# Kernel tuning notes

Hardware: AMD Instinct MI355X
Metric: run time of the kernel (lower is better)

## Reference

```python
import jax, jax.numpy as jnp
import numpy as np

N, E, H, OUT, L = 50000, 500000, 256, 128, 2
EPS = 1e-5  # torch LayerNorm default


def _make_edges(k):
    # both rows cover all N nodes so that unique()/remap in the original is identity
    k1, k2, kp = jax.random.split(k, 3)
    row0 = jnp.concatenate([jax.random.permutation(kp, N), jax.random.randint(k1, (E - N,), 0, N)])
    row1 = jnp.concatenate([jnp.arange(N), jax.random.randint(k2, (E - N,), 0, N)])
    return jnp.stack([row0, row1]).astype(jnp.int32)


def setup_inputs() -> dict:
    key = jax.random.key(0)
    ks = jax.random.split(key, 7)
    s = 0.02
    x = jax.random.normal(ks[0], (N, H), jnp.float32)
    edge_r1 = _make_edges(ks[1])
    edge_r2 = _make_edges(ks[2])
    Wl = jax.random.normal(ks[3], (L, H, H), jnp.float32) * s
    W0 = jax.random.normal(ks[4], (L, H, H), jnp.float32) * s
    W1 = jax.random.normal(ks[5], (L, H, H), jnp.float32) * s
    bl = jnp.zeros((L, H), jnp.float32)
    b0 = jnp.zeros((L, H), jnp.float32)
    b1 = jnp.zeros((L, H), jnp.float32)
    gamma = jnp.ones((L, H), jnp.float32)
    beta = jnp.zeros((L, H), jnp.float32)
    Wout = jax.random.normal(ks[6], (OUT, H), jnp.float32) * s
    bout = jnp.zeros((OUT,), jnp.float32)
    return dict(x=x, edge_r1=edge_r1, edge_r2=edge_r2, Wl=Wl, bl=bl, W0=W0, b0=b0,
                W1=W1, b1=b1, gamma=gamma, beta=beta, Wout=Wout, bout=bout)


def _layer(i, h, x0, e, Wl, bl, W0, b0, W1, b1, gamma, beta):
    # PyG flow='target_to_source', aggr='add': gather h at e[1], scatter-add at e[0]
    agg = jax.ops.segment_sum(h[e[1]], e[0], num_segments=h.shape[0])  # [N, H]
    z = agg @ Wl[i].T + bl[i] + h @ W0[i].T + b0[i] + x0 @ W1[i].T + b1[i]
    z = jax.nn.relu(z)
    mu = jnp.mean(z, axis=-1, keepdims=True)
    var = jnp.mean(jnp.square(z - mu), axis=-1, keepdims=True)
    return (z - mu) * jax.lax.rsqrt(var + EPS) * gamma[i] + beta[i]  # dropout is identity in eval


def reference(x, edge_r1, edge_r2, Wl, bl, W0, b0, W1, b1, gamma, beta, Wout, bout):
    # reversed(metapath): (C,r2,C) with conv_idx=1 first, then (C,r1,C) with conv_idx=0
    h = _layer(1, x, x, edge_r2, Wl, bl, W0, b0, W1, b1, gamma, beta)
    h = _layer(0, h, x, edge_r1, Wl, bl, W0, b0, W1, b1, gamma, beta)
    return h @ Wout.T + bout  # [N, OUT]
```

## Files before the change

### kernel.cpp

```cpp
#include <hip/hip_runtime.h>
#include <stdint.h>

#define N_NODES 50000
#define N_EDGES 500000
#define NPAD    50048
#define NBLK    128
#define EPB     4096
#define NBUCK   391
#define LFLAT   50048
#define NSC2    196
#define P4CAP   4096
#define EPS     1e-5f

typedef _Float16 half8_ __attribute__((ext_vector_type(8)));
typedef _Float16 half4_ __attribute__((ext_vector_type(4)));
typedef float    float4_ __attribute__((ext_vector_type(4)));

typedef uint32_t u32_g __attribute__((address_space(1)));
typedef uint32_t u32_s __attribute__((address_space(3)));

__device__ __forceinline__ void gload16(const void* g, void* lds_wave_base) {
    __builtin_amdgcn_global_load_lds((const u32_g*)g, (u32_s*)lds_wave_base, 16, 0, 0);
}

__global__ __launch_bounds__(256) void prep_kernel(
        const int* __restrict__ e1, const int* __restrict__ e2,
        int* __restrict__ G, unsigned short* __restrict__ rank16,
        const float* __restrict__ x, _Float16* __restrict__ xh,
        _Float16* __restrict__ aggb, _Float16* __restrict__ h1,
        const float* __restrict__ Wl, const float* __restrict__ W0,
        const float* __restrict__ W1, const float* __restrict__ Wout,
        _Float16* __restrict__ Wcat,
        const float* __restrict__ bl, const float* __restrict__ b0,
        const float* __restrict__ b1, const float* __restrict__ bout,
        float* __restrict__ bias) {
    __shared__ int hist[NBUCK];
    const int bid = blockIdx.x;
    const int tid = threadIdx.x;
    if (bid < 256) {
        const int s = bid >> 7, blk = bid & 127;
        const int* dst = s ? e2 : e1;
        unsigned short* rk = rank16 + (size_t)s * N_EDGES;
        for (int b = tid; b < NBUCK; b += 256) hist[b] = 0;
        __syncthreads();
        const int e0 = blk * EPB;
        int myrank[16];
#pragma unroll
        for (int k = 0; k < 16; k++) {
            int i = e0 + k * 256 + tid;
            int r = 0;
            if (i < N_EDGES) r = atomicAdd(&hist[dst[i] >> 7], 1);
            myrank[k] = r;
        }
#pragma unroll
        for (int k = 0; k < 16; k++) {
            int i = e0 + k * 256 + tid;
            if (i < N_EDGES) rk[i] = (unsigned short)myrank[k];
        }
        __syncthreads();
        int* Gp = G + (s * NBLK + blk) * NBUCK;
        for (int b = tid; b < NBUCK; b += 256) Gp[b] = hist[b];
    } else if (bid < 12756) {
        int i = (bid - 256) * 256 + tid;
        float4_ v = ((const float4_*)x)[i];
        half4_ h;
        h[0] = (_Float16)v[0]; h[1] = (_Float16)v[1];
        h[2] = (_Float16)v[2]; h[3] = (_Float16)v[3];
        ((half4_*)xh)[i] = h;
    } else if (bid < 14420) {
        int i = (bid - 12756) * 256 + tid;
        if (i < 2 * 256 * 768) {
            int l = i / (256 * 768);
            int r = i % (256 * 768);
            int j = r / 768, k = r % 768;
            const float* s = (k < 256) ? Wl : (k < 512 ? W0 : W1);
            Wcat[i] = (_Float16)s[l * 65536 + j * 256 + (k & 255)];
        } else {
            Wcat[i] = (_Float16)Wout[i - 2 * 256 * 768];
        }
    } else if (bid < 14456) {
        int j = (bid - 14420) * 256 + tid;
        int buf = j / 3072, jj = j % 3072;
        _Float16* p = (buf == 0) ? xh : (buf == 1) ? aggb : h1;
        half4_ z = {(_Float16)0.f, (_Float16)0.f, (_Float16)0.f, (_Float16)0.f};
        *(half4_*)(p + (size_t)N_NODES * 256 + (size_t)jj * 4) = z;
    } else {
        int i = (bid - 14456) * 256 + tid;
        if (i < 512)      bias[i] = bl[i] + b0[i] + b1[i];
        else if (i < 640) bias[i] = bout[i - 512];
    }
}

__global__ __launch_bounds__(256) void p2_scan(const int* __restrict__ G,
                                               unsigned long long* __restrict__ state,
                                               int* __restrict__ start2) {
    __shared__ int sm[256];
    __shared__ int s_excl;
    const int bid = blockIdx.x;
    const int s = bid / NSC2;
    const int seq = bid % NSC2;
    const int t = threadIdx.x;
    const int i = seq * 256 + t;
    unsigned long long* st = state + s * NSC2;

    int v = 0;
    if (i < LFLAT) v = G[(s * NBLK + (i & 127)) * NBUCK + (i >> 7)];
    sm[t] = v;
    __syncthreads();
    for (int off = 1; off < 256; off <<= 1) {
        int x = sm[t];
        if (t >= off) x += sm[t - off];
        __syncthreads();
        sm[t] = x;
        __syncthreads();
    }
    int total = sm[255];

    if (t == 0) {
        if (seq == 0) {
            atomicExch(&st[0], (2ULL << 32) | (unsigned int)total);
            s_excl = 0;
        } else {
            atomicExch(&st[seq], (1ULL << 32) | (unsigned int)total);
            int running = 0;
            int j = seq - 1;
            while (true) {
                unsigned long long sv = atomicAdd(&st[j], 0ULL);
                unsigned int tag = (unsigned int)(sv >> 32);
                if (tag == 0) continue;
                running += (int)(unsigned int)sv;
                if (tag == 2) break;
                j--;
            }
            atomicExch(&st[seq], (2ULL << 32) | (unsigned int)(running + total));
            s_excl = running;
        }
    }
    __syncthreads();
    if (i < LFLAT) start2[s * LFLAT + i] = s_excl + sm[t] - v;
}

__global__ __launch_bounds__(256) void p3_scatter(const int* __restrict__ e1,
                                                  const int* __restrict__ e2,
                                                  const unsigned short* __restrict__ rank16,
                                                  const int* __restrict__ start2,
                                                  unsigned int* __restrict__ tmp) {
    const int bid = blockIdx.x;
    const int s = bid >> 7, blk = bid & 127;
    const int t = threadIdx.x;
    const int* ed = s ? e2 : e1;
    const int* st = start2 + s * LFLAT;
    const unsigned short* rk = rank16 + (size_t)s * N_EDGES;
    unsigned int* tp = tmp + (size_t)s * N_EDGES;
    const int e0 = blk * EPB;
#pragma unroll
    for (int k = 0; k < 16; k++) {
        int i = e0 + k * 256 + t;
        if (i < N_EDGES) {
            int d   = ed[i];
            int src = ed[N_EDGES + i];
            int pos = st[(d >> 7) * NBLK + blk] + (int)rk[i];
            tp[pos] = ((unsigned)(d & 127) << 16) | (unsigned)src;
        }
    }
}

__global__ __launch_bounds__(256) void p4_build(const unsigned int* __restrict__ tmp,
                                                const int* __restrict__ start2,
                                                int* __restrict__ rp,
                                                int* __restrict__ col) {
    __shared__ int cnt[128];
    __shared__ int off[128];
    __shared__ unsigned int   stM[P4CAP];
    __shared__ unsigned short stS[P4CAP];
    const int b = blockIdx.x;
    const int s = blockIdx.y;
    const int t = threadIdx.x;
    const int* st = start2 + s * LFLAT;
    const int A   = st[b * NBLK];
    const int Bnd = (b == NBUCK - 1) ? N_EDGES : st[(b + 1) * NBLK];
    const unsigned int* tp = tmp + (size_t)s * N_EDGES;

    if (t < 128) cnt[t] = 0;
    __syncthreads();
    for (int eb = A; eb < Bnd; eb += 256) {
        int e = eb + t;
        if (e < Bnd) {
            unsigned v = tp[e];
            int idx = (int)(v >> 16);
            int r = atomicAdd(&cnt[idx], 1);
            int sl = e - A;
            if (sl < P4CAP) {
                stM[sl] = ((unsigned)idx << 12) | (unsigned)r;
                stS[sl] = (unsigned short)(v & 0xFFFFu);
            }
        }
    }
    __syncthreads();
    if (t < 128) off[t] = cnt[t];
    __syncthreads();
    for (int d = 1; d < 128; d <<= 1) {
        int x = 0;
        if (t < 128) { x = off[t]; if (t >= d) x += off[t - d]; }
        __syncthreads();
        if (t < 128) off[t] = x;
        __syncthreads();
    }
    const int nE = Bnd - A;
    int* colS = col + (size_t)s * N_EDGES;
    for (int sl = t; sl < nE && sl < P4CAP; sl += 256) {
        unsigned m = stM[sl];
        int idx = (int)(m >> 12), r = (int)(m & 4095u);
        colS[A + off[idx] - cnt[idx] + r] = (int)stS[sl];
    }
    const int nbase = b * 128;
    if (t < 128 && nbase + t < N_NODES)
        rp[s * (N_NODES + 1) + nbase + t] = A + off[t] - cnt[t];
    if (b == NBUCK - 1 && t == 0) rp[s * (N_NODES + 1) + N_NODES] = N_EDGES;
}

__global__ void gather_kernel(const _Float16* __restrict__ hin,
                              const int* __restrict__ rowptr, const int* __restrict__ col,
                              _Float16* __restrict__ dst, int n) {
    int node = blockIdx.x * 4 + (threadIdx.x >> 6);
    int lane = threadIdx.x & 63;
    int half = lane >> 5, l5 = lane & 31;
    if (node >= n) return;
    int s = rowptr[node], e = rowptr[node + 1];
    float a[8] = {0.f, 0.f, 0.f, 0.f, 0.f, 0.f, 0.f, 0.f};
    float b[8] = {0.f, 0.f, 0.f, 0.f, 0.f, 0.f, 0.f, 0.f};
    int i = s + half;
    for (; i + 6 < e; i += 8) {
        int c0 = col[i], c1 = col[i + 2], c2 = col[i + 4], c3 = col[i + 6];
        half8_ v0 = *(const half8_*)(hin + (size_t)c0 * 256 + l5 * 8);
        half8_ v1 = *(const half8_*)(hin + (size_t)c1 * 256 + l5 * 8);
        half8_ v2 = *(const half8_*)(hin + (size_t)c2 * 256 + l5 * 8);
        half8_ v3 = *(const half8_*)(hin + (size_t)c3 * 256 + l5 * 8);
#pragma unroll
        for (int j = 0; j < 8; j++) {
            a[j] += (float)v0[j] + (float)v2[j];
            b[j] += (float)v1[j] + (float)v3[j];
        }
    }
    for (; i < e; i += 2) {
        int c0 = col[i];
        half8_ v0 = *(const half8_*)(hin + (size_t)c0 * 256 + l5 * 8);
#pragma unroll
        for (int j = 0; j < 8; j++) a[j] += (float)v0[j];
    }
    half8_ o;
#pragma unroll
    for (int j = 0; j < 8; j++) {
        float t = a[j] + b[j];
        t += __shfl_xor(t, 32, 64);
        o[j] = (_Float16)t;
    }
    if (half == 0)
        *(half8_*)(dst + (size_t)node * 256 + l5 * 8) = o;
}

__global__ __launch_bounds__(512) void gemm_ln(const _Float16* __restrict__ agg,
                                               const _Float16* __restrict__ hsrc,
                                               const _Float16* __restrict__ xh,
                                               const _Float16* __restrict__ Bw,
                                               const float* __restrict__ bias,
                                               const float* __restrict__ gamma,
                                               const float* __restrict__ beta,
                                               _Float16* __restrict__ H) {
    __shared__ __align__(16) char smem[49152];
    char* AsB = smem;
    char* BsB = smem + 16384;
    const int rowBase = blockIdx.x * 128;
    const int tid  = threadIdx.x;
    const int lane = tid & 63;
    const int w    = tid >> 6;
    const int wm = w & 1, wn = w >> 1;
    const int quad = lane >> 4, mr = lane & 15;
    const int x7 = mr & 7;

    float4_ acc[4][4];
#pragma unroll
    for (int i = 0; i < 4; i++)
#pragma unroll
        for (int j = 0; j < 4; j++) { float4_ z4 = {0.f, 0.f, 0.f, 0.f}; acc[i][j] = z4; }

    int cA0 = w * 64 + lane, cA1 = cA0 + 512;
    int rA0 = cA0 >> 3, rA1 = cA1 >> 3;
    size_t offA0 = (size_t)(rowBase + rA0) * 256 + (((cA0 & 7) ^ (rA0 & 7)) * 8);
    size_t offA1 = (size_t)(rowBase + rA1) * 256 + (((cA1 & 7) ^ (rA1 & 7)) * 8);
    size_t offB[4];
#pragma unroll
    for (int j = 0; j < 4; j++) {
        int c = j * 512 + w * 64 + lane;
        int r = c >> 3;
        offB[j] = (size_t)r * 768 + (((c & 7) ^ (r & 7)) * 8);
    }
    void* lA0 = AsB + w * 1024;
    void* lA1 = AsB + 8192 + w * 1024;

    for (int k0 = 0; k0 < 768; k0 += 64) {
        const _Float16* src = (k0 < 256) ? agg : (k0 < 512) ? hsrc : xh;
        const int kloc = k0 & 255;
        gload16(src + offA0 + kloc, lA0);
        gload16(src + offA1 + kloc, lA1);
        gload16(Bw + offB[0] + k0, BsB + w * 1024);
        gload16(Bw + offB[1] + k0, BsB + 8192 + w * 1024);
        gload16(Bw + offB[2] + k0, BsB + 16384 + w * 1024);
        gload16(Bw + offB[3] + k0, BsB + 24576 + w * 1024);
        __syncthreads();
#pragma unroll
        for (int s = 0; s < 2; s++) {
            half8_ a[4], b[4];
#pragma unroll
            for (int im = 0; im < 4; im++) {
                int row = wm * 64 + im * 16 + mr;
                a[im] = *(const half8_*)(AsB + row * 128 + (((s * 4 + quad) ^ x7) * 16));
            }
#pragma unroll
            for (int in = 0; in < 4; in++) {
                int row = wn * 64 + in * 16 + mr;
                b[in] = *(const half8_*)(BsB + row * 128 + (((s * 4 + quad) ^ x7) * 16));
            }
#pragma unroll
            for (int im = 0; im < 4; im++)
#pragma unroll
                for (int in = 0; in < 4; in++)
                    acc[im][in] = __builtin_amdgcn_mfma_f32_16x16x32_f16(a[im], b[in], acc[im][in], 0, 0, 0);
        }
        __syncthreads();
    }

    float bv[4], gv[4], bev[4];
#pragma unroll
    for (int in = 0; in < 4; in++) {
        int colg = wn * 64 + in * 16 + mr;
        bv[in]  = bias[colg];
        gv[in]  = gamma[colg];
        bev[in] = beta[colg];
    }
    float* lnbuf   = (float*)AsB;
    float* lnstats = (float*)(AsB + 4096);

#pragma unroll
    for (int im = 0; im < 4; im++)
#pragma unroll
        for (int r = 0; r < 4; r++) {
            float s = 0.f, sq = 0.f;
#pragma unroll
            for (int in = 0; in < 4; in++) {
                float v = acc[im][in][r] + bv[in];
                v = v > 0.f ? v : 0.f;
                s += v; sq += v * v;
            }
            s  += __shfl_xor(s, 1, 64);  sq += __shfl_xor(sq, 1, 64);
            s  += __shfl_xor(s, 2, 64);  sq += __shfl_xor(sq, 2, 64);
            s  += __shfl_xor(s, 4, 64);  sq += __shfl_xor(sq, 4, 64);
            s  += __shfl_xor(s, 8, 64);  sq += __shfl_xor(sq, 8, 64);
            if (mr == 0) {
                int rl = wm * 64 + im * 16 + quad * 4 + r;
                lnbuf[(wn * 128 + rl) * 2]     = s;
                lnbuf[(wn * 128 + rl) * 2 + 1] = sq;
            }
        }
    __syncthreads();
    if (tid < 128) {
        float s  = lnbuf[tid * 2]             + lnbuf[(128 + tid) * 2]
                 + lnbuf[(256 + tid) * 2]     + lnbuf[(384 + tid) * 2];
        float sq = lnbuf[tid * 2 + 1]         + lnbuf[(128 + tid) * 2 + 1]
                 + lnbuf[(256 + tid) * 2 + 1] + lnbuf[(384 + tid) * 2 + 1];
        float mu  = s * (1.0f / 256.0f);
        float var = sq * (1.0f / 256.0f) - mu * mu;
        lnstats[tid * 2]     = mu;
        lnstats[tid * 2 + 1] = rsqrtf(var + EPS);
    }
    __syncthreads();

    _Float16* BsH = (_Float16*)BsB;
#pragma unroll
    for (int p = 0; p < 2; p++) {
        if (wm == p) {
#pragma unroll
            for (int im = 0; im < 4; im++)
#pragma unroll
                for (int r = 0; r < 4; r++) {
                    int rl = im * 16 + quad * 4 + r;
                    float mu = lnstats[(p * 64 + rl) * 2];
                    float rs = lnstats[(p * 64 + rl) * 2 + 1];
#pragma unroll
                    for (int in = 0; in < 4; in++) {
                        float v = acc[im][in][r] + bv[in];
                        v = v > 0.f ? v : 0.f;
                        BsH[rl * 256 + wn * 64 + in * 16 + mr] =
                            (_Float16)((v - mu) * rs * gv[in] + bev[in]);
                    }
                }
        }
        __syncthreads();
#pragma unroll
        for (int i = 0; i < 4; i++) {
            int c = i * 512 + tid;
            int row = c >> 5, ch = c & 31;
            half8_ v = *(const half8_*)(BsB + c * 16);
            *(half8_*)(H + (size_t)(rowBase + p * 64 + row) * 256 + ch * 8) = v;
        }
        __syncthreads();
    }
}

__global__ __launch_bounds__(256) void gemm_bt(const _Float16* __restrict__ A, int lda,
                                               const _Float16* __restrict__ B, int ldb,
                                               const float* __restrict__ bias,
                                               float* __restrict__ C, int ldc,
                                               int K, int Mstore) {
    __shared__ _Float16 As[128 * 32];
    __shared__ _Float16 Bs[128 * 32];
    const int rowBase = blockIdx.x * 128;
    const int colBase = blockIdx.y * 128;
    const int tid  = threadIdx.x;
    const int lane = tid & 63;
    const int w    = tid >> 6;
    const int wm = w & 1, wn = w >> 1;
    const int quad = lane >> 4, mr = lane & 15;

    float4_ acc[4][4];
#pragma unroll
    for (int i = 0; i < 4; i++)
#pragma unroll
        for (int j = 0; j < 4; j++) { float4_ z4 = {0.f, 0.f, 0.f, 0.f}; acc[i][j] = z4; }

    const int c0  = w * 64 + lane;
    const int rA0 = c0 >> 2;
    const int ko  = (c0 & 3) * 8;
    char* AsB = (char*)As;
    char* BsB = (char*)Bs;
    void* lA0 = AsB + w * 1024;
    void* lA1 = AsB + 4096 + w * 1024;
    void* lB0 = BsB + w * 1024;
    void* lB1 = BsB + 4096 + w * 1024;
    const _Float16* gA0 = A + (size_t)(rowBase + rA0) * lda + ko;
    const _Float16* gA1 = gA0 + (size_t)64 * lda;
    const _Float16* gB0 = B + (size_t)(colBase + rA0) * ldb + ko;
    const _Float16* gB1 = gB0 + (size_t)64 * ldb;

    for (int k0 = 0; k0 < K; k0 += 32) {
        gload16(gA0 + k0, lA0);
        gload16(gA1 + k0, lA1);
        gload16(gB0 + k0, lB0);
        gload16(gB1 + k0, lB1);
        __syncthreads();
        half8_ a[4], b[4];
#pragma unroll
        for (int im = 0; im < 4; im++)
            a[im] = *(const half8_*)(AsB + ((wm * 64 + im * 16 + mr) * 64 + quad * 16));
#pragma unroll
        for (int in = 0; in < 4; in++)
            b[in] = *(const half8_*)(BsB + ((wn * 64 + in * 16 + mr) * 64 + quad * 16));
#pragma unroll
        for (int im = 0; im < 4; im++)
#pragma unroll
            for (int in = 0; in < 4; in++)
                acc[im][in] = __builtin_amdgcn_mfma_f32_16x16x32_f16(a[im], b[in], acc[im][in], 0, 0, 0);
        __syncthreads();
    }

#pragma unroll
    for (int in = 0; in < 4; in++) {
        const int colg = colBase + wn * 64 + in * 16 + mr;
        const float bv = bias[colg];
#pragma unroll
        for (int im = 0; im < 4; im++) {
            float4_ c = acc[im][in];
#pragma unroll
            for (int r = 0; r < 4; r++) {
                int row = rowBase + wm * 64 + im * 16 + quad * 4 + r;
                if (row < Mstore) C[(size_t)row * ldc + colg] = c[r] + bv;
            }
        }
    }
}

extern "C" void kernel_launch(void* const* d_in, const int* in_sizes, int n_in,
                              void* d_out, int out_size, void* d_ws, size_t ws_size,
                              hipStream_t stream) {
    const float* x    = (const float*)d_in[0];
    const int*   e1   = (const int*)d_in[1];
    const int*   e2   = (const int*)d_in[2];
    const float* Wl   = (const float*)d_in[3];
    const float* bl   = (const float*)d_in[4];
    const float* W0   = (const float*)d_in[5];
    const float* b0   = (const float*)d_in[6];
    const float* W1   = (const float*)d_in[7];
    const float* b1   = (const float*)d_in[8];
    const float* gamma= (const float*)d_in[9];
    const float* beta = (const float*)d_in[10];
    const float* Wout = (const float*)d_in[11];
    const float* bout = (const float*)d_in[12];

    char* ws = (char*)d_ws;
    size_t off = 0;
    auto alloc = [&](size_t bytes) -> char* {
        char* p = ws + off;
        off = (off + bytes + 255) & ~(size_t)255;
        return p;
    };
    _Float16* xh   = (_Float16*)alloc((size_t)NPAD * 256 * 2);
    _Float16* aggb = (_Float16*)alloc((size_t)NPAD * 256 * 2);
    _Float16* h1   = (_Float16*)alloc((size_t)NPAD * 256 * 2);
    _Float16* h2   = (_Float16*)alloc((size_t)NPAD * 256 * 2);
    _Float16* Wcat = (_Float16*)alloc((size_t)(2 * 256 * 768 + 128 * 256) * 2);
    float*    bias = (float*)alloc(640 * 4);
    unsigned long long* states = (unsigned long long*)alloc((size_t)2 * NSC2 * 8);
    int* G      = (int*)alloc((size_t)2 * NBLK * NBUCK * 4);
    int* start2 = (int*)alloc((size_t)2 * LFLAT * 4);
    int* rp     = (int*)alloc((size_t)2 * (N_NODES + 1) * 4);
    unsigned short* rank16 = (unsigned short*)alloc((size_t)2 * N_EDGES * 2);
    unsigned int*   tmp    = (unsigned int*)alloc((size_t)2 * N_EDGES * 4);
    int* col    = (int*)alloc((size_t)2 * N_EDGES * 4);

    int* rp1 = rp, *rp2 = rp + (N_NODES + 1);
    int* col1 = col, *col2 = col + N_EDGES;

    hipMemsetAsync(states, 0, (size_t)2 * NSC2 * 8, stream);

    prep_kernel<<<14459, 256, 0, stream>>>(e1, e2, G, rank16, x, xh, aggb, h1,
                                           Wl, W0, W1, Wout, Wcat,
                                           bl, b0, b1, bout, bias);
    p2_scan<<<2 * NSC2, 256, 0, stream>>>(G, states, start2);
    p3_scatter<<<256, 256, 0, stream>>>(e1, e2, rank16, start2, tmp);
    p4_build<<<dim3(NBUCK, 2), 256, 0, stream>>>(tmp, start2, rp, col);

    const int nb4 = (N_NODES + 3) / 4;
    const _Float16* WoutH = Wcat + 393216;

    gather_kernel<<<nb4, 256, 0, stream>>>(xh, rp2, col2, aggb, N_NODES);
    gemm_ln<<<391, 512, 0, stream>>>(aggb, xh, xh, Wcat + 196608,
                                     bias + 256, gamma + 256, beta + 256, h1);
    gather_kernel<<<nb4, 256, 0, stream>>>(h1, rp1, col1, aggb, N_NODES);
    gemm_ln<<<391, 512, 0, stream>>>(aggb, h1, xh, Wcat,
                                     bias, gamma, beta, h2);
    gemm_bt<<<dim3(391, 1), 256, 0, stream>>>(h2, 256, WoutH, 256,
                                              bias + 512, (float*)d_out, 128, 256, N_NODES);
}
```

Baseline: 321.2 us.

## Merge CSR build phases into one cooperative kernel with grid syncs

Fuses the prep, scan, scatter and build kernels plus the state memset into a single cooperative kernel of 1024 persistent blocks. Grid-wide syncs separate the phases, and a grid-stride loop over virtual block IDs replaces the separate launches. This removes several kernel launch gaps and the memset, at the cost of grid.sync overhead and less parallelism in phases that ran many blocks before. It also relies on all 1024 blocks with about 25KB of LDS each being co-resident.

Result: slower. 969.0 us (+201.7%).

```diff
diff --git a/kernel.cpp b/kernel.cpp
--- a/kernel.cpp
+++ b/kernel.cpp
@@ -1,5 +1,8 @@
 #include <hip/hip_runtime.h>
+#include <hip/hip_cooperative_groups.h>
 #include <stdint.h>
+
+namespace cg = cooperative_groups;
 
 #define N_NODES 50000
 #define N_EDGES 500000
@@ -10,6 +13,7 @@
 #define LFLAT   50048
 #define NSC2    196
 #define P4CAP   4096
+#define NB      1024
 #define EPS     1e-5f
 
 typedef _Float16 half8_ __attribute__((ext_vector_type(8)));
@@ -23,7 +27,7 @@
     __builtin_amdgcn_global_load_lds((const u32_g*)g, (u32_s*)lds_wave_base, 16, 0, 0);
 }
 
-__global__ __launch_bounds__(256) void prep_kernel(
+__global__ __launch_bounds__(256) void build_all(
         const int* __restrict__ e1, const int* __restrict__ e2,
         int* __restrict__ G, unsigned short* __restrict__ rank16,
         const float* __restrict__ x, _Float16* __restrict__ xh,
@@ -33,190 +37,196 @@
         _Float16* __restrict__ Wcat,
         const float* __restrict__ bl, const float* __restrict__ b0,
         const float* __restrict__ b1, const float* __restrict__ bout,
-        float* __restrict__ bias) {
-    __shared__ int hist[NBUCK];
+        float* __restrict__ bias,
+        unsigned long long* __restrict__ states,
+        int* __restrict__ start2, unsigned int* __restrict__ tmp,
+        int* __restrict__ rp, int* __restrict__ col) {
+    __shared__ __align__(16) char uls[25856];
+    cg::grid_group grid = cg::this_grid();
     const int bid = blockIdx.x;
     const int tid = threadIdx.x;
+
+    for (int vb = bid; vb < 14460; vb += NB) {
+        if (vb < 256) {
+            int* hist = (int*)uls;
+            const int s = vb >> 7, blk = vb & 127;
+            const int* dst = s ? e2 : e1;
+            unsigned short* rk = rank16 + (size_t)s * N_EDGES;
+            for (int b = tid; b < NBUCK; b += 256) hist[b] = 0;
+            __syncthreads();
+            const int e0 = blk * EPB;
+            int myrank[16];
+#pragma unroll
+            for (int k = 0; k < 16; k++) {
+                int i = e0 + k * 256 + tid;
+                int r = 0;
+                if (i < N_EDGES) r = atomicAdd(&hist[dst[i] >> 7], 1);
+                myrank[k] = r;
+            }
+#pragma unroll
+            for (int k = 0; k < 16; k++) {
+                int i = e0 + k * 256 + tid;
+                if (i < N_EDGES) rk[i] = (unsigned short)myrank[k];
+            }
+            __syncthreads();
+            int* Gp = G + (s * NBLK + blk) * NBUCK;
+            for (int b = tid; b < NBUCK; b += 256) Gp[b] = hist[b];
+            __syncthreads();
+        } else if (vb < 12756) {
+            int i = (vb - 256) * 256 + tid;
+            float4_ v = ((const float4_*)x)[i];
+            half4_ h;
+            h[0] = (_Float16)v[0]; h[1] = (_Float16)v[1];
+            h[2] = (_Float16)v[2]; h[3] = (_Float16)v[3];
+            ((half4_*)xh)[i] = h;
+        } else if (vb < 14420) {
+            int i = (vb - 12756) * 256 + tid;
+            if (i < 2 * 256 * 768) {
+                int l = i / (256 * 768);
+                int r = i % (256 * 768);
+                int j = r / 768, k = r % 768;
+                const float* s = (k < 256) ? Wl : (k < 512 ? W0 : W1);
+                Wcat[i] = (_Float16)s[l * 65536 + j * 256 + (k & 255)];
+            } else {
+                Wcat[i] = (_Float16)Wout[i - 2 * 256 * 768];
+            }
+        } else if (vb < 14456) {
+            int j = (vb - 14420) * 256 + tid;
+            int buf = j / 3072, jj = j % 3072;
+            _Float16* p = (buf == 0) ? xh : (buf == 1) ? aggb : h1;
+            half4_ z = {(_Float16)0.f, (_Float16)0.f, (_Float16)0.f, (_Float16)0.f};
+            *(half4_*)(p + (size_t)N_NODES * 256 + (size_t)jj * 4) = z;
+        } else if (vb < 14459) {
+            int i = (vb - 14456) * 256 + tid;
+            if (i < 512)      bias[i] = bl[i] + b0[i] + b1[i];
+            else if (i < 640) bias[i] = bout[i - 512];
+        } else {
+            for (int i = tid; i < 2 * NSC2; i += 256) states[i] = 0ULL;
+        }
+    }
+    __threadfence();
+    grid.sync();
+
+    if (bid < 2 * NSC2) {
+        int* sm = (int*)uls;
+        int* s_excl = (int*)(uls + 1024);
+        const int s = bid / NSC2;
+        const int seq = bid % NSC2;
+        const int t = tid;
+        const int i = seq * 256 + t;
+        unsigned long long* st = states + s * NSC2;
+
+        int v = 0;
+        if (i < LFLAT) v = G[(s * NBLK + (i & 127)) * NBUCK + (i >> 7)];
+        sm[t] = v;
+        __syncthreads();
+        for (int off = 1; off < 256; off <<= 1) {
+            int xv = sm[t];
+            if (t >= off) xv += sm[t - off];
+            __syncthreads();
+            sm[t] = xv;
+            __syncthreads();
+        }
+        int total = sm[255];
+
+        if (t == 0) {
+            if (seq == 0) {
+                atomicExch(&st[0], (2ULL << 32) | (unsigned int)total);
+                *s_excl = 0;
+            } else {
+                atomicExch(&st[seq], (1ULL << 32) | (unsigned int)total);
+                int running = 0;
+                int j = seq - 1;
+                while (true) {
+                    unsigned long long sv = atomicAdd(&st[j], 0ULL);
+                    unsigned int tag = (unsigned int)(sv >> 32);
+                    if (tag == 0) continue;
+                    running += (int)(unsigned int)sv;
+                    if (tag == 2) break;
+                    j--;
+                }
+                atomicExch(&st[seq], (2ULL << 32) | (unsigned int)(running + total));
+                *s_excl = running;
+            }
+        }
+        __syncthreads();
+        if (i < LFLAT) start2[s * LFLAT + i] = *s_excl + sm[t] - v;
+    }
+    __threadfence();
+    grid.sync();
+
     if (bid < 256) {
         const int s = bid >> 7, blk = bid & 127;
-        const int* dst = s ? e2 : e1;
-        unsigned short* rk = rank16 + (size_t)s * N_EDGES;
-        for (int b = tid; b < NBUCK; b += 256) hist[b] = 0;
-        __syncthreads();
+        const int* ed = s ? e2 : e1;
+        const int* st = start2 + s * LFLAT;
+        const unsigned short* rk = rank16 + (size_t)s * N_EDGES;
+        unsigned int* tp = tmp + (size_t)s * N_EDGES;
         const int e0 = blk * EPB;
-        int myrank[16];
 #pragma unroll
         for (int k = 0; k < 16; k++) {
             int i = e0 + k * 256 + tid;
-            int r = 0;
-            if (i < N_EDGES) r = atomicAdd(&hist[dst[i] >> 7], 1);
-            myrank[k] = r;
-        }
-#pragma unroll
-        for (int k = 0; k < 16; k++) {
-            int i = e0 + k * 256 + tid;
-            if (i < N_EDGES) rk[i] = (unsigned short)myrank[k];
-        }
-        __syncthreads();
-        int* Gp = G + (s * NBLK + blk) * NBUCK;
-        for (int b = tid; b < NBUCK; b += 256) Gp[b] = hist[b];
-    } else if (bid < 12756) {
-        int i = (bid - 256) * 256 + tid;
-        float4_ v = ((const float4_*)x)[i];
-        half4_ h;
-        h[0] = (_Float16)v[0]; h[1] = (_Float16)v[1];
-        h[2] = (_Float16)v[2]; h[3] = (_Float16)v[3];
-        ((half4_*)xh)[i] = h;
-    } else if (bid < 14420) {
-        int i = (bid - 12756) * 256 + tid;
-        if (i < 2 * 256 * 768) {
-            int l = i / (256 * 768);
-            int r = i % (256 * 768);
-            int j = r / 768, k = r % 768;
-            const float* s = (k < 256) ? Wl : (k < 512 ? W0 : W1);
-            Wcat[i] = (_Float16)s[l * 65536 + j * 256 + (k & 255)];
-        } else {
-            Wcat[i] = (_Float16)Wout[i - 2 * 256 * 768];
-        }
-    } else if (bid < 14456) {
-        int j = (bid - 14420) * 256 + tid;
-        int buf = j / 3072, jj = j % 3072;
-        _Float16* p = (buf == 0) ? xh : (buf == 1) ? aggb : h1;
-        half4_ z = {(_Float16)0.f, (_Float16)0.f, (_Float16)0.f, (_Float16)0.f};
-        *(half4_*)(p + (size_t)N_NODES * 256 + (size_t)jj * 4) = z;
-    } else {
-        int i = (bid - 14456) * 256 + tid;
-        if (i < 512)      bias[i] = bl[i] + b0[i] + b1[i];
-        else if (i < 640) bias[i] = bout[i - 512];
-    }
-}
-
-__global__ __launch_bounds__(256) void p2_scan(const int* __restrict__ G,
-                                               unsigned long long* __restrict__ state,
-                                               int* __restrict__ start2) {
-    __shared__ int sm[256];
-    __shared__ int s_excl;
-    const int bid = blockIdx.x;
-    const int s = bid / NSC2;
-    const int seq = bid % NSC2;
-    const int t = threadIdx.x;
-    const int i = seq * 256 + t;
-    unsigned long long* st = state + s * NSC2;
-
-    int v = 0;
-    if (i < LFLAT) v = G[(s * NBLK + (i & 127)) * NBUCK + (i >> 7)];
-    sm[t] = v;
-    __syncthreads();
-    for (int off = 1; off < 256; off <<= 1) {
-        int x = sm[t];
-        if (t >= off) x += sm[t - off];
-        __syncthreads();
-        sm[t] = x;
-        __syncthreads();
-    }
-    int total = sm[255];
-
-    if (t == 0) {
-        if (seq == 0) {
-            atomicExch(&st[0], (2ULL << 32) | (unsigned int)total);
-            s_excl = 0;
-        } else {
-            atomicExch(&st[seq], (1ULL << 32) | (unsigned int)total);
-            int running = 0;
-            int j = seq - 1;
-            while (true) {
-                unsigned long long sv = atomicAdd(&st[j], 0ULL);
-                unsigned int tag = (unsigned int)(sv >> 32);
-                if (tag == 0) continue;
-                running += (int)(unsigned int)sv;
-                if (tag == 2) break;
-                j--;
-            }
-            atomicExch(&st[seq], (2ULL << 32) | (unsigned int)(running + total));
-            s_excl = running;
-        }
-    }
-    __syncthreads();
-    if (i < LFLAT) start2[s * LFLAT + i] = s_excl + sm[t] - v;
-}
-
-__global__ __launch_bounds__(256) void p3_scatter(const int* __restrict__ e1,
-                                                  const int* __restrict__ e2,
-                                                  const unsigned short* __restrict__ rank16,
-                                                  const int* __restrict__ start2,
-                                                  unsigned int* __restrict__ tmp) {
-    const int bid = blockIdx.x;
-    const int s = bid >> 7, blk = bid & 127;
-    const int t = threadIdx.x;
-    const int* ed = s ? e2 : e1;
-    const int* st = start2 + s * LFLAT;
-    const unsigned short* rk = rank16 + (size_t)s * N_EDGES;
-    unsigned int* tp = tmp + (size_t)s * N_EDGES;
-    const int e0 = blk * EPB;
-#pragma unroll
-    for (int k = 0; k < 16; k++) {
-        int i = e0 + k * 256 + t;
-        if (i < N_EDGES) {
-            int d   = ed[i];
-            int src = ed[N_EDGES + i];
-            int pos = st[(d >> 7) * NBLK + blk] + (int)rk[i];
-            tp[pos] = ((unsigned)(d & 127) << 16) | (unsigned)src;
-        }
-    }
-}
-
-__global__ __launch_bounds__(256) void p4_build(const unsigned int* __restrict__ tmp,
-                                                const int* __restrict__ start2,
-                                                int* __restrict__ rp,
-                                                int* __restrict__ col) {
-    __shared__ int cnt[128];
-    __shared__ int off[128];
-    __shared__ unsigned int   stM[P4CAP];
-    __shared__ unsigned short stS[P4CAP];
-    const int b = blockIdx.x;
-    const int s = blockIdx.y;
-    const int t = threadIdx.x;
-    const int* st = start2 + s * LFLAT;
-    const int A   = st[b * NBLK];
-    const int Bnd = (b == NBUCK - 1) ? N_EDGES : st[(b + 1) * NBLK];
-    const unsigned int* tp = tmp + (size_t)s * N_EDGES;
-
-    if (t < 128) cnt[t] = 0;
-    __syncthreads();
-    for (int eb = A; eb < Bnd; eb += 256) {
-        int e = eb + t;
-        if (e < Bnd) {
-            unsigned v = tp[e];
-            int idx = (int)(v >> 16);
-            int r = atomicAdd(&cnt[idx], 1);
-            int sl = e - A;
-            if (sl < P4CAP) {
-                stM[sl] = ((unsigned)idx << 12) | (unsigned)r;
-                stS[sl] = (unsigned short)(v & 0xFFFFu);
-            }
-        }
-    }
-    __syncthreads();
-    if (t < 128) off[t] = cnt[t];
-    __syncthreads();
-    for (int d = 1; d < 128; d <<= 1) {
-        int x = 0;
-        if (t < 128) { x = off[t]; if (t >= d) x += off[t - d]; }
-        __syncthreads();
-        if (t < 128) off[t] = x;
-        __syncthreads();
-    }
-    const int nE = Bnd - A;
-    int* colS = col + (size_t)s * N_EDGES;
-    for (int sl = t; sl < nE && sl < P4CAP; sl += 256) {
-        unsigned m = stM[sl];
-        int idx = (int)(m >> 12), r = (int)(m & 4095u);
-        colS[A + off[idx] - cnt[idx] + r] = (int)stS[sl];
-    }
-    const int nbase = b * 128;
-    if (t < 128 && nbase + t < N_NODES)
-        rp[s * (N_NODES + 1) + nbase + t] = A + off[t] - cnt[t];
-    if (b == NBUCK - 1 && t == 0) rp[s * (N_NODES + 1) + N_NODES] = N_EDGES;
+            if (i < N_EDGES) {
+                int d   = ed[i];
+                int src = ed[N_EDGES + i];
+                int pos = st[(d >> 7) * NBLK + blk] + (int)rk[i];
+                tp[pos] = ((unsigned)(d & 127) << 16) | (unsigned)src;
+            }
+        }
+    }
+    __threadfence();
+    grid.sync();
+
+    for (int vb = bid; vb < 2 * NBUCK; vb += NB) {
+        int* cnt = (int*)uls;
+        int* off = (int*)(uls + 512);
+        unsigned int*   stM = (unsigned int*)(uls + 1024);
+        unsigned short* stS = (unsigned short*)(uls + 1024 + 16384);
+        const int s = vb / NBUCK;
+        const int b = vb - s * NBUCK;
+        const int t = tid;
+        const int* st = start2 + s * LFLAT;
+        const int A   = st[b * NBLK];
+        const int Bnd = (b == NBUCK - 1) ? N_EDGES : st[(b + 1) * NBLK];
+        const unsigned int* tp = tmp + (size_t)s * N_EDGES;
+
+        if (t < 128) cnt[t] = 0;
+        __syncthreads();
+        for (int eb = A; eb < Bnd; eb += 256) {
+            int e = eb + t;
+            if (e < Bnd) {
+                unsigned v = tp[e];
+                int idx = (int)(v >> 16);
+                int r = atomicAdd(&cnt[idx], 1);
+                int sl = e - A;
+                if (sl < P4CAP) {
+                    stM[sl] = ((unsigned)idx << 12) | (unsigned)r;
+                    stS[sl] = (unsigned short)(v & 0xFFFFu);
+                }
+            }
+        }
+        __syncthreads();
+        if (t < 128) off[t] = cnt[t];
+        __syncthreads();
+        for (int d = 1; d < 128; d <<= 1) {
+            int xv = 0;
+            if (t < 128) { xv = off[t]; if (t >= d) xv += off[t - d]; }
+            __syncthreads();
+            if (t < 128) off[t] = xv;
+            __syncthreads();
+        }
+        const int nE = Bnd - A;
+        int* colS = col + (size_t)s * N_EDGES;
+        for (int sl = t; sl < nE && sl < P4CAP; sl += 256) {
+            unsigned m = stM[sl];
+            int idx = (int)(m >> 12), r = (int)(m & 4095u);
+            colS[A + off[idx] - cnt[idx] + r] = (int)stS[sl];
+        }
+        const int nbase = b * 128;
+        if (t < 128 && nbase + t < N_NODES)
+            rp[s * (N_NODES + 1) + nbase + t] = A + off[t] - cnt[t];
+        if (b == NBUCK - 1 && t == 0) rp[s * (N_NODES + 1) + N_NODES] = N_EDGES;
+        __syncthreads();
+    }
 }
 
 __global__ void gather_kernel(const _Float16* __restrict__ hin,
@@ -520,14 +530,15 @@
     int* rp1 = rp, *rp2 = rp + (N_NODES + 1);
     int* col1 = col, *col2 = col + N_EDGES;
 
-    hipMemsetAsync(states, 0, (size_t)2 * NSC2 * 8, stream);
-
-    prep_kernel<<<14459, 256, 0, stream>>>(e1, e2, G, rank16, x, xh, aggb, h1,
-                                           Wl, W0, W1, Wout, Wcat,
-                                           bl, b0, b1, bout, bias);
-    p2_scan<<<2 * NSC2, 256, 0, stream>>>(G, states, start2);
-    p3_scatter<<<256, 256, 0, stream>>>(e1, e2, rank16, start2, tmp);
-    p4_build<<<dim3(NBUCK, 2), 256, 0, stream>>>(tmp, start2, rp, col);
+    void* kargs[] = {
+        (void*)&e1, (void*)&e2, (void*)&G, (void*)&rank16,
+        (void*)&x, (void*)&xh, (void*)&aggb, (void*)&h1,
+        (void*)&Wl, (void*)&W0, (void*)&W1, (void*)&Wout, (void*)&Wcat,
+        (void*)&bl, (void*)&b0, (void*)&b1, (void*)&bout, (void*)&bias,
+        (void*)&states, (void*)&start2, (void*)&tmp, (void*)&rp, (void*)&col
+    };
+    hipLaunchCooperativeKernel((const void*)build_all, dim3(NB), dim3(256),
+                               kargs, 0, stream);
 
     const int nb4 = (N_NODES + 3) / 4;
     const _Float16* WoutH = Wcat + 393216;
```
